# Kernel tuning notes

Hardware: AMD Instinct MI355X
Metric: run time of the kernel (lower is better)

Reference implementation:

```python
import jax, jax.numpy as jnp
import numpy as np

N, M, K = 100000, 20000, 640000   # nodes, hyperedges, incidence entries
IN_DIM, HID = 256, 128
L = 3                             # hdn_layers
EPS = 1e-5                        # BatchNorm1d eps


def setup_inputs() -> dict:
    key = jax.random.key(0)
    ks = jax.random.split(key, 8)
    init = lambda k, shape, fan: jax.random.normal(k, shape, jnp.float32) * (1.0 / np.sqrt(fan))
    return {
        "X": jax.random.normal(ks[0], (N, IN_DIM), jnp.float32),
        "node_idx": jax.random.randint(ks[1], (K,), 0, N, jnp.int32),
        "edge_idx": jax.random.randint(ks[2], (K,), 0, M, jnp.int32),
        "hyperedge_weight": jax.random.uniform(ks[3], (M,), jnp.float32),
        "W_up": init(ks[4], (IN_DIM, HID), IN_DIM),
        "b_up": jnp.zeros((HID,), jnp.float32),
        "bn_gamma": jnp.ones((L, HID), jnp.float32),
        "bn_beta": jnp.zeros((L, HID), jnp.float32),
        "W_conv": init(ks[5], (L, HID, HID), HID),
        "b_conv": jnp.zeros((L, HID), jnp.float32),
        "W_gate": init(ks[6], (L, HID, 1), HID),
        "b_gate": jnp.zeros((L, 1), jnp.float32),  # init_bias = 0.0
    }


def _batchnorm(x, gamma, beta):
    # BatchNorm1d in training mode: batch stats, biased variance
    mu = jnp.mean(x, axis=0)
    var = jnp.mean(jnp.square(x - mu), axis=0)
    return (x - mu) * jax.lax.rsqrt(var + EPS) * gamma + beta


def _hypergraph_conv(x, W, b, node_idx, edge_idx, w):
    # PyG HypergraphConv (heads=1): X' = D^{-1} H B^{-1} H^T (X W) + b,
    # where D_i = sum_{e ni i} w_e (w enters only via D, per PyG source),
    # B_e = |e|. 1/0 -> 0 as in PyG.
    x = x @ W                                                   # [N, HID]
    D = jax.ops.segment_sum(w[edge_idx], node_idx, num_segments=N)
    Dinv = jnp.where(D > 0, 1.0 / D, 0.0)
    Bdeg = jax.ops.segment_sum(jnp.ones((K,), x.dtype), edge_idx, num_segments=M)
    Binv = jnp.where(Bdeg > 0, 1.0 / Bdeg, 0.0)
    e = jax.ops.segment_sum(x[node_idx], edge_idx, num_segments=M) * Binv[:, None]   # edge feats [M, HID]
    out = jax.ops.segment_sum(e[edge_idx], node_idx, num_segments=N) * Dinv[:, None]  # node feats [N, HID]
    return out + b


def reference(X, node_idx, edge_idx, hyperedge_weight, W_up, b_up,
              bn_gamma, bn_beta, W_conv, b_conv, W_gate, b_gate):
    # lin_up: Linear + ReLU (in_dim != hidden_dim)
    x = jax.nn.relu(X @ W_up + b_up)
    identity = x
    for i in range(L):
        h = jax.nn.relu(_hypergraph_conv(
            _batchnorm(x, bn_gamma[i], bn_beta[i]),
            W_conv[i], b_conv[i], node_idx, edge_idx, hyperedge_weight))
        gate = jax.nn.sigmoid(x @ W_gate[i] + b_gate[i])        # [N, 1]
        x = x + h * gate
    # hidden_dim == out_dim -> lin_down = Identity, conv_down = Identity
    return (x + identity) + x
```

## Files before the change

kernel.cpp:

```cpp
#include <hip/hip_runtime.h>
#include <math.h>

#define NN 100000
#define MM 20000
#define KINC 640000
#define INDIM 256
#define HIDDIM 128
#define EPSBN 1e-5f

typedef __attribute__((ext_vector_type(4))) float f32x4;
typedef __attribute__((ext_vector_type(8))) short bf16x8;
typedef unsigned short ushort_t;

__device__ inline unsigned f2bf_bits(float f) {
  unsigned u = __float_as_uint(f);
  return u + 0x7FFFu + ((u >> 16) & 1u);
}
__device__ inline void split1(float f, ushort_t& hi, ushort_t& lo) {
  unsigned rh = f2bf_bits(f) & 0xFFFF0000u;
  hi = (ushort_t)(rh >> 16);
  float d = f - __uint_as_float(rh);
  lo = (ushort_t)(f2bf_bits(d) >> 16);
}


__global__ void hist_kernel(const int* __restrict__ nidx, const int* __restrict__ eidx,
                            const float* __restrict__ w, int* __restrict__ ecnt,
                            int* __restrict__ ncnt, float* __restrict__ D) {
  int stride = gridDim.x * blockDim.x;
  for (int k = blockIdx.x * blockDim.x + threadIdx.x; k < KINC; k += stride) {
    int e = eidx[k], n = nidx[k];
    atomicAdd(&ecnt[e], 1);
    atomicAdd(&ncnt[n], 1);
    atomicAdd(&D[n], w[e]);
  }
}

__global__ void base_kernel(const int* __restrict__ cnt, int* __restrict__ ptr,
                            int* __restrict__ pend, float* __restrict__ binv,
                            int* __restrict__ counter, int len) {
  int i = blockIdx.x * blockDim.x + threadIdx.x;
  int lane = threadIdx.x & 63;
  int v = (i < len) ? cnt[i] : 0;
  int s = v;
  #pragma unroll
  for (int off = 1; off < 64; off <<= 1) {
    int t = __shfl_up(s, off);
    if (lane >= off) s += t;
  }
  int total = __shfl(s, 63);
  int base = 0;
  if (lane == 0) base = atomicAdd(counter, total);
  base = __shfl(base, 0);
  if (i < len) {
    ptr[i] = base + s - v;
    pend[i] = base + s;
    if (binv) binv[i] = (v > 0) ? 1.0f / (float)v : 0.0f;
  }
}

__global__ void fill_kernel(const int* __restrict__ nidx, const int* __restrict__ eidx,
                            int* __restrict__ ecnt, int* __restrict__ ncnt,
                            const int* __restrict__ eptr, const int* __restrict__ nptr,
                            int* __restrict__ enodes, int* __restrict__ nedges) {
  int stride = gridDim.x * blockDim.x;
  for (int k = blockIdx.x * blockDim.x + threadIdx.x; k < KINC; k += stride) {
    int e = eidx[k], n = nidx[k];
    int pe = atomicSub(&ecnt[e], 1) - 1;
    enodes[eptr[e] + pe] = n;
    int pn = atomicSub(&ncnt[n], 1) - 1;
    nedges[nptr[n] + pn] = e;
  }
}

__global__ void dinv_kernel(float* __restrict__ D) {
  int i = blockIdx.x * blockDim.x + threadIdx.x;
  if (i < NN) { float d = D[i]; D[i] = (d > 0.0f) ? 1.0f / d : 0.0f; }
}

__global__ void wsplit_up_kernel(const float* __restrict__ W, ushort_t* __restrict__ Th,
                                 ushort_t* __restrict__ Tl) {
  int idx = blockIdx.x * 256 + threadIdx.x;
  int c = idx >> 8, k = idx & 255;
  ushort_t h, l;
  split1(W[k * HIDDIM + c], h, l);
  Th[c * INDIM + k] = h;
  Tl[c * INDIM + k] = l;
}

__global__ void prep_kernel(const float* __restrict__ stats, const float* __restrict__ gamma,
    const float* __restrict__ beta, const float* __restrict__ Wc,
    ushort_t* __restrict__ Th, ushort_t* __restrict__ Tl, float* __restrict__ bp) {
  __shared__ float al[128], cc[128];
  int t = threadIdx.x;
  if (t < 128) {
    float mu = stats[t] * (1.0f / NN);
    float var = fmaxf(stats[128 + t] * (1.0f / NN) - mu * mu, 0.0f);
    float a = gamma[t] * rsqrtf(var + EPSBN);
    al[t] = a;
    cc[t] = beta[t] - mu * a;
  }
  __syncthreads();
  for (int idx = t; idx < 128 * 128; idx += 256) {
    int c = idx >> 7, k = idx & 127;
    ushort_t h, l;
    split1(al[k] * Wc[k * 128 + c], h, l);
    Th[c * 128 + k] = h;
    Tl[c * 128 + k] = l;
  }
  if (t < 128) {
    float b = 0.f;
    for (int k = 0; k < 128; ++k) b = fmaf(cc[k], Wc[k * 128 + t], b);
    bp[t] = b;
  }
}

template<int KDIM, bool RELU, bool DUP>
__global__ __launch_bounds__(256) void mgemm_kernel(const float* __restrict__ A,
    const ushort_t* __restrict__ BTh, const ushort_t* __restrict__ BTl,
    const float* __restrict__ bias, float* __restrict__ out, float* __restrict__ out2,
    int nrows) {
  const int lane = threadIdx.x & 63;
  const int wv = threadIdx.x >> 6;
  const int m = lane & 15;
  const int kg = lane >> 4;
  const int r0 = blockIdx.x * 128;
  const int rt0 = r0 + wv * 16;
  const int rt1 = r0 + 64 + wv * 16;

  f32x4 acc0[8], acc1[8];
  #pragma unroll
  for (int ct = 0; ct < 8; ++ct) {
    acc0[ct] = (f32x4){0.f, 0.f, 0.f, 0.f};
    acc1[ct] = (f32x4){0.f, 0.f, 0.f, 0.f};
  }
  float bv[8];
  #pragma unroll
  for (int ct = 0; ct < 8; ++ct) bv[ct] = bias[ct * 16 + m];

  const int row0 = rt0 + m, row1 = rt1 + m;
  const bool v0 = row0 < nrows, v1 = row1 < nrows;
  const float* a0p = A + (size_t)row0 * KDIM + kg * 8;
  const float* a1p = A + (size_t)row1 * KDIM + kg * 8;

  for (int ks = 0; ks < KDIM; ks += 32) {
    float a0[8] = {0, 0, 0, 0, 0, 0, 0, 0}, a1[8] = {0, 0, 0, 0, 0, 0, 0, 0};
    if (v0) {
      *(float4*)(a0) = *(const float4*)(a0p + ks);
      *(float4*)(a0 + 4) = *(const float4*)(a0p + ks + 4);
    }
    if (v1) {
      *(float4*)(a1) = *(const float4*)(a1p + ks);
      *(float4*)(a1 + 4) = *(const float4*)(a1p + ks + 4);
    }
    bf16x8 a0h, a0l, a1h, a1l;
    #pragma unroll
    for (int j = 0; j < 8; ++j) {
      ushort_t h, l;
      split1(a0[j], h, l); a0h[j] = (short)h; a0l[j] = (short)l;
      split1(a1[j], h, l); a1h[j] = (short)h; a1l[j] = (short)l;
    }
    #pragma unroll
    for (int ct = 0; ct < 8; ++ct) {
      size_t bo = (size_t)(ct * 16 + m) * KDIM + ks + kg * 8;
      bf16x8 bh = *(const bf16x8*)(BTh + bo);
      bf16x8 bl = *(const bf16x8*)(BTl + bo);
      acc0[ct] = __builtin_amdgcn_mfma_f32_16x16x32_bf16(a0h, bh, acc0[ct], 0, 0, 0);
      acc0[ct] = __builtin_amdgcn_mfma_f32_16x16x32_bf16(a0l, bh, acc0[ct], 0, 0, 0);
      acc0[ct] = __builtin_amdgcn_mfma_f32_16x16x32_bf16(a0h, bl, acc0[ct], 0, 0, 0);
      acc1[ct] = __builtin_amdgcn_mfma_f32_16x16x32_bf16(a1h, bh, acc1[ct], 0, 0, 0);
      acc1[ct] = __builtin_amdgcn_mfma_f32_16x16x32_bf16(a1l, bh, acc1[ct], 0, 0, 0);
      acc1[ct] = __builtin_amdgcn_mfma_f32_16x16x32_bf16(a1h, bl, acc1[ct], 0, 0, 0);
    }
  }
  #pragma unroll
  for (int ct = 0; ct < 8; ++ct) {
    #pragma unroll
    for (int j = 0; j < 4; ++j) {
      int r = rt0 + kg * 4 + j;
      if (r < nrows) {
        float v = acc0[ct][j] + bv[ct];
        if (RELU) v = fmaxf(v, 0.0f);
        out[(size_t)r * HIDDIM + ct * 16 + m] = v;
        if (DUP) out2[(size_t)r * HIDDIM + ct * 16 + m] = v;
      }
      r = rt1 + kg * 4 + j;
      if (r < nrows) {
        float v = acc1[ct][j] + bv[ct];
        if (RELU) v = fmaxf(v, 0.0f);
        out[(size_t)r * HIDDIM + ct * 16 + m] = v;
        if (DUP) out2[(size_t)r * HIDDIM + ct * 16 + m] = v;
      }
    }
  }
}

__global__ __launch_bounds__(256) void stats_kernel(const float* __restrict__ x,
    float* __restrict__ out, int n) {
  __shared__ float lsum[128], lsq[128];
  int t = threadIdx.x;
  int lane = t & 63, wv = t >> 6;
  if (t < 128) { lsum[t] = 0.f; lsq[t] = 0.f; }
  __syncthreads();
  float sx = 0, sy = 0, qx = 0, qy = 0;
  const float2* x2 = (const float2*)x;
  for (int r = blockIdx.x * 4 + wv; r < n; r += gridDim.x * 4) {
    float2 v = x2[(size_t)r * 64 + lane];
    sx += v.x; sy += v.y; qx += v.x * v.x; qy += v.y * v.y;
  }
  atomicAdd(&lsum[2 * lane], sx);
  atomicAdd(&lsum[2 * lane + 1], sy);
  atomicAdd(&lsq[2 * lane], qx);
  atomicAdd(&lsq[2 * lane + 1], qy);
  __syncthreads();
  if (t < 128) {
    atomicAdd(&out[t], lsum[t]);
    atomicAdd(&out[128 + t], lsq[t]);
  }
}

__global__ __launch_bounds__(256) void edge_agg_kernel(const float* __restrict__ xw,
    const int* __restrict__ eptr, const int* __restrict__ pend,
    const int* __restrict__ enodes, const float* __restrict__ binv,
    float* __restrict__ e2) {
  int gw = (blockIdx.x * 256 + threadIdx.x) >> 6;
  int lane = threadIdx.x & 63;
  int e = __builtin_amdgcn_readfirstlane(gw);
  if (e >= MM) return;
  int p0 = eptr[e], p1 = pend[e];
  const float2* xw2 = (const float2*)xw;
  float ax = 0, ay = 0, bx = 0, by = 0;
  int j = p0;
  for (; j + 2 <= p1; j += 2) {
    int n0 = enodes[j], n1 = enodes[j + 1];
    float2 v0 = xw2[(size_t)n0 * 64 + lane];
    float2 v1 = xw2[(size_t)n1 * 64 + lane];
    ax += v0.x; ay += v0.y; bx += v1.x; by += v1.y;
  }
  if (j < p1) {
    int n0 = enodes[j];
    float2 v0 = xw2[(size_t)n0 * 64 + lane];
    ax += v0.x; ay += v0.y;
  }
  float bi = binv[e];
  float2 r; r.x = (ax + bx) * bi; r.y = (ay + by) * bi;
  ((float2*)e2)[(size_t)e * 64 + lane] = r;
}

template<bool LAST>
__global__ __launch_bounds__(256) void node_agg_kernel(const float* __restrict__ e2,
    const int* __restrict__ nptr, const int* __restrict__ pend,
    const int* __restrict__ nedges, const float* __restrict__ dinv,
    const float* __restrict__ bconv, const float* __restrict__ wgate,
    const float* __restrict__ bgate, const float* __restrict__ x,
    float* __restrict__ xout, const float* __restrict__ idres, float* __restrict__ fout,
    float* __restrict__ stats_out) {
  __shared__ float ls[256];
  int t = threadIdx.x;
  int lane = t & 63, wv = t >> 6;
  ls[t] = 0.f;
  __syncthreads();
  float sx = 0, sy = 0, qx = 0, qy = 0;
  const float2* e22 = (const float2*)e2;
  for (int nid0 = blockIdx.x * 4 + wv; nid0 < NN; nid0 += gridDim.x * 4) {
    int nid = __builtin_amdgcn_readfirstlane(nid0);
    int p0 = nptr[nid], p1 = pend[nid];
    float ax = 0, ay = 0;
    for (int j = p0; j < p1; ++j) {
      int e = nedges[j];
      float2 v = e22[(size_t)e * 64 + lane];
      ax += v.x; ay += v.y;
    }
    float di = dinv[nid];
    float2 xv = ((const float2*)x)[(size_t)nid * 64 + lane];
    float2 wg = ((const float2*)wgate)[lane];
    float part = xv.x * wg.x + xv.y * wg.y;
    #pragma unroll
    for (int off = 32; off >= 1; off >>= 1) part += __shfl_xor(part, off);
    float g = 1.0f / (1.0f + expf(-(part + bgate[0])));
    float2 bc = ((const float2*)bconv)[lane];
    float hx = fmaxf(fmaf(ax, di, bc.x), 0.0f);
    float hy = fmaxf(fmaf(ay, di, bc.y), 0.0f);
    float2 xn; xn.x = fmaf(hx, g, xv.x); xn.y = fmaf(hy, g, xv.y);
    if (LAST) {
      float2 idv = ((const float2*)idres)[(size_t)nid * 64 + lane];
      float2 o; o.x = 2.0f * xn.x + idv.x; o.y = 2.0f * xn.y + idv.y;
      ((float2*)fout)[(size_t)nid * 64 + lane] = o;
    } else {
      ((float2*)xout)[(size_t)nid * 64 + lane] = xn;
      sx += xn.x; sy += xn.y; qx += xn.x * xn.x; qy += xn.y * xn.y;
    }
  }
  if (!LAST) {
    atomicAdd(&ls[2 * lane], sx);
    atomicAdd(&ls[2 * lane + 1], sy);
    atomicAdd(&ls[128 + 2 * lane], qx);
    atomicAdd(&ls[128 + 2 * lane + 1], qy);
    __syncthreads();
    atomicAdd(&stats_out[t], ls[t]);
  }
}

extern "C" void kernel_launch(void* const* d_in, const int* in_sizes, int n_in,
                              void* d_out, int out_size, void* d_ws, size_t ws_size,
                              hipStream_t stream) {
  const float* X      = (const float*)d_in[0];
  const int*   nidx   = (const int*)d_in[1];
  const int*   eidx   = (const int*)d_in[2];
  const float* hw     = (const float*)d_in[3];
  const float* W_up   = (const float*)d_in[4];
  const float* b_up   = (const float*)d_in[5];
  const float* gamma  = (const float*)d_in[6];
  const float* beta   = (const float*)d_in[7];
  const float* W_conv = (const float*)d_in[8];
  const float* b_conv = (const float*)d_in[9];
  const float* W_gate = (const float*)d_in[10];
  const float* b_gate = (const float*)d_in[11];
  float* out = (float*)d_out;

  char* ws = (char*)d_ws;
  size_t off = 0;
  auto alloc = [&](size_t bytes) -> void* {
    void* p = ws + off;
    off = (off + bytes + 255) & ~(size_t)255;
    return p;
  };
  float* D     = (float*)alloc((size_t)NN * 4);
  int*   ecnt  = (int*)alloc((size_t)MM * 4);
  int*   ncnt  = (int*)alloc((size_t)NN * 4);
  int*   ctrs  = (int*)alloc(256);
  float* stats = (float*)alloc(3 * 256 * 4);
  size_t zero_bytes = off;
  int*   eptr   = (int*)alloc((size_t)MM * 4);
  int*   epend  = (int*)alloc((size_t)MM * 4);
  int*   nptr   = (int*)alloc((size_t)NN * 4);
  int*   npend  = (int*)alloc((size_t)NN * 4);
  float* Binv   = (float*)alloc((size_t)MM * 4);
  int*   enodes = (int*)alloc((size_t)KINC * 4);
  int*   nedges = (int*)alloc((size_t)KINC * 4);
  float* x      = (float*)alloc((size_t)NN * HIDDIM * 4);
  float* idr    = (float*)alloc((size_t)NN * HIDDIM * 4);
  float* e2     = (float*)alloc((size_t)MM * HIDDIM * 4);
  ushort_t* WupTh = (ushort_t*)alloc((size_t)HIDDIM * INDIM * 2);
  ushort_t* WupTl = (ushort_t*)alloc((size_t)HIDDIM * INDIM * 2);
  ushort_t* WTh   = (ushort_t*)alloc((size_t)HIDDIM * HIDDIM * 2);
  ushort_t* WTl   = (ushort_t*)alloc((size_t)HIDDIM * HIDDIM * 2);
  float* bp     = (float*)alloc((size_t)HIDDIM * 4);
  float* xw     = out;

  hipMemsetAsync(d_ws, 0, zero_bytes, stream);
  hist_kernel<<<512, 256, 0, stream>>>(nidx, eidx, hw, ecnt, ncnt, D);
  base_kernel<<<(MM + 255) / 256, 256, 0, stream>>>(ecnt, eptr, epend, Binv, ctrs + 0, MM);
  base_kernel<<<(NN + 255) / 256, 256, 0, stream>>>(ncnt, nptr, npend, nullptr, ctrs + 1, NN);
  fill_kernel<<<512, 256, 0, stream>>>(nidx, eidx, ecnt, ncnt, eptr, nptr, enodes, nedges);
  dinv_kernel<<<(NN + 255) / 256, 256, 0, stream>>>(D);
  wsplit_up_kernel<<<128, 256, 0, stream>>>(W_up, WupTh, WupTl);

  mgemm_kernel<INDIM, true, true><<<(NN + 127) / 128, 256, 0, stream>>>(
      X, WupTh, WupTl, b_up, x, idr, NN);
  stats_kernel<<<256, 256, 0, stream>>>(x, stats + 0, NN);

  for (int i = 0; i < 3; ++i) {
    prep_kernel<<<1, 256, 0, stream>>>(stats + i * 256, gamma + i * 128, beta + i * 128,
                                       W_conv + (size_t)i * 128 * 128, WTh, WTl, bp);
    mgemm_kernel<HIDDIM, false, false><<<(NN + 127) / 128, 256, 0, stream>>>(
        x, WTh, WTl, bp, xw, nullptr, NN);
    edge_agg_kernel<<<MM / 4, 256, 0, stream>>>(xw, eptr, epend, enodes, Binv, e2);
    if (i < 2)
      node_agg_kernel<false><<<1280, 256, 0, stream>>>(e2, nptr, npend, nedges, D,
          b_conv + i * 128, W_gate + i * 128, b_gate + i, x, x, nullptr, nullptr,
          stats + (i + 1) * 256);
    else
      node_agg_kernel<true><<<1280, 256, 0, stream>>>(e2, nptr, npend, nedges, D,
          b_conv + i * 128, W_gate + i * 128, b_gate + i, x, nullptr, idr, out, nullptr);
  }
}
```

Baseline: 1.042 ms.

## Pre-swizzle split weights into MFMA fragment order and stage them in LDS

Weight hi/lo bf16 splits are now written in MFMA fragment order, so each lane's 8-element operand is contiguous. The GEMM copies 64-K chunks of these fragments into shared memory before use instead of re-reading them from global memory per tile. The operands are swapped so the output tile is transposed, which lets each lane store rows as float4. Blocks now cover 64 rows instead of 128 with 4-block occupancy hints, trading per-wave A-row reuse for more parallelism and adding block barriers.

```diff
diff --git a/kernel.cpp b/kernel.cpp
--- a/kernel.cpp
+++ b/kernel.cpp
@@ -78,19 +78,26 @@
   if (i < NN) { float d = D[i]; D[i] = (d > 0.0f) ? 1.0f / d : 0.0f; }
 }
 
-__global__ void wsplit_up_kernel(const float* __restrict__ W, ushort_t* __restrict__ Th,
-                                 ushort_t* __restrict__ Tl) {
-  int idx = blockIdx.x * 256 + threadIdx.x;
-  int c = idx >> 8, k = idx & 255;
-  ushort_t h, l;
-  split1(W[k * HIDDIM + c], h, l);
-  Th[c * INDIM + k] = h;
-  Tl[c * INDIM + k] = l;
+__global__ void wsplit_up_kernel(const float* __restrict__ W, ushort_t* __restrict__ Fh,
+                                 ushort_t* __restrict__ Fl) {
+  int g = blockIdx.x * 256 + threadIdx.x;
+  int ln = g & 63;
+  int ct = (g >> 6) & 7;
+  int ksg = g >> 9;
+  int c = ct * 16 + (ln & 15);
+  int k0 = ksg * 32 + (ln >> 4) * 8;
+  #pragma unroll
+  for (int j = 0; j < 8; ++j) {
+    ushort_t h, l;
+    split1(W[(size_t)(k0 + j) * HIDDIM + c], h, l);
+    Fh[(size_t)g * 8 + j] = h;
+    Fl[(size_t)g * 8 + j] = l;
+  }
 }
 
 __global__ void prep_kernel(const float* __restrict__ stats, const float* __restrict__ gamma,
     const float* __restrict__ beta, const float* __restrict__ Wc,
-    ushort_t* __restrict__ Th, ushort_t* __restrict__ Tl, float* __restrict__ bp) {
+    ushort_t* __restrict__ Fh, ushort_t* __restrict__ Fl, float* __restrict__ bp) {
   __shared__ float al[128], cc[128];
   int t = threadIdx.x;
   if (t < 128) {
@@ -101,12 +108,19 @@
     cc[t] = beta[t] - mu * a;
   }
   __syncthreads();
-  for (int idx = t; idx < 128 * 128; idx += 256) {
-    int c = idx >> 7, k = idx & 127;
-    ushort_t h, l;
-    split1(al[k] * Wc[k * 128 + c], h, l);
-    Th[c * 128 + k] = h;
-    Tl[c * 128 + k] = l;
+  for (int g = t; g < 2048; g += 256) {
+    int ln = g & 63;
+    int ct = (g >> 6) & 7;
+    int ksg = g >> 9;
+    int c = ct * 16 + (ln & 15);
+    int k0 = ksg * 32 + (ln >> 4) * 8;
+    #pragma unroll
+    for (int j = 0; j < 8; ++j) {
+      ushort_t h, l;
+      split1(al[k0 + j] * Wc[(k0 + j) * 128 + c], h, l);
+      Fh[(size_t)g * 8 + j] = h;
+      Fl[(size_t)g * 8 + j] = l;
+    }
   }
   if (t < 128) {
     float b = 0.f;
@@ -116,81 +130,81 @@
 }
 
 template<int KDIM, bool RELU, bool DUP>
-__global__ __launch_bounds__(256) void mgemm_kernel(const float* __restrict__ A,
-    const ushort_t* __restrict__ BTh, const ushort_t* __restrict__ BTl,
+__global__ __launch_bounds__(256, 4) void mgemm_kernel(const float* __restrict__ A,
+    const ushort_t* __restrict__ WFh, const ushort_t* __restrict__ WFl,
     const float* __restrict__ bias, float* __restrict__ out, float* __restrict__ out2,
     int nrows) {
-  const int lane = threadIdx.x & 63;
-  const int wv = threadIdx.x >> 6;
+  __shared__ ushort_t Bls[16384];
+  const int t = threadIdx.x;
+  const int lane = t & 63;
+  const int wv = t >> 6;
   const int m = lane & 15;
   const int kg = lane >> 4;
-  const int r0 = blockIdx.x * 128;
-  const int rt0 = r0 + wv * 16;
-  const int rt1 = r0 + 64 + wv * 16;
-
-  f32x4 acc0[8], acc1[8];
+  const int rt = blockIdx.x * 64 + wv * 16;
+
+  f32x4 acc[8];
   #pragma unroll
-  for (int ct = 0; ct < 8; ++ct) {
-    acc0[ct] = (f32x4){0.f, 0.f, 0.f, 0.f};
-    acc1[ct] = (f32x4){0.f, 0.f, 0.f, 0.f};
-  }
-  float bv[8];
-  #pragma unroll
-  for (int ct = 0; ct < 8; ++ct) bv[ct] = bias[ct * 16 + m];
-
-  const int row0 = rt0 + m, row1 = rt1 + m;
-  const bool v0 = row0 < nrows, v1 = row1 < nrows;
+  for (int ct = 0; ct < 8; ++ct) acc[ct] = (f32x4){0.f, 0.f, 0.f, 0.f};
+
+  const int row0 = rt + m;
+  const bool v0 = row0 < nrows;
   const float* a0p = A + (size_t)row0 * KDIM + kg * 8;
-  const float* a1p = A + (size_t)row1 * KDIM + kg * 8;
-
-  for (int ks = 0; ks < KDIM; ks += 32) {
-    float a0[8] = {0, 0, 0, 0, 0, 0, 0, 0}, a1[8] = {0, 0, 0, 0, 0, 0, 0, 0};
-    if (v0) {
-      *(float4*)(a0) = *(const float4*)(a0p + ks);
-      *(float4*)(a0 + 4) = *(const float4*)(a0p + ks + 4);
-    }
-    if (v1) {
-      *(float4*)(a1) = *(const float4*)(a1p + ks);
-      *(float4*)(a1 + 4) = *(const float4*)(a1p + ks + 4);
-    }
-    bf16x8 a0h, a0l, a1h, a1l;
-    #pragma unroll
-    for (int j = 0; j < 8; ++j) {
-      ushort_t h, l;
-      split1(a0[j], h, l); a0h[j] = (short)h; a0l[j] = (short)l;
-      split1(a1[j], h, l); a1h[j] = (short)h; a1l[j] = (short)l;
-    }
+
+  for (int c2 = 0; c2 < KDIM / 64; ++c2) {
+    if (c2) __syncthreads();
+    const uint4* sh = (const uint4*)(WFh + c2 * 8192);
+    const uint4* sl = (const uint4*)(WFl + c2 * 8192);
+    uint4* dh = (uint4*)Bls;
+    uint4* dl = (uint4*)(Bls + 8192);
+    #pragma unroll
+    for (int i = 0; i < 4; ++i) {
+      dh[i * 256 + t] = sh[i * 256 + t];
+      dl[i * 256 + t] = sl[i * 256 + t];
+    }
+    __syncthreads();
+    #pragma unroll
+    for (int ks2 = 0; ks2 < 2; ++ks2) {
+      int kof = c2 * 64 + ks2 * 32;
+      float a0[8] = {0, 0, 0, 0, 0, 0, 0, 0};
+      if (v0) {
+        *(float4*)(a0) = *(const float4*)(a0p + kof);
+        *(float4*)(a0 + 4) = *(const float4*)(a0p + kof + 4);
+      }
+      bf16x8 a0h, a0l;
+      #pragma unroll
+      for (int j = 0; j < 8; ++j) {
+        ushort_t h, l;
+        split1(a0[j], h, l);
+        a0h[j] = (short)h;
+        a0l[j] = (short)l;
+      }
+      #pragma unroll
+      for (int ct = 0; ct < 8; ++ct) {
+        int fo = ((ks2 * 8 + ct) * 64 + lane) * 8;
+        bf16x8 bh = *(const bf16x8*)(Bls + fo);
+        bf16x8 bl = *(const bf16x8*)(Bls + 8192 + fo);
+        acc[ct] = __builtin_amdgcn_mfma_f32_16x16x32_bf16(bh, a0h, acc[ct], 0, 0, 0);
+        acc[ct] = __builtin_amdgcn_mfma_f32_16x16x32_bf16(bl, a0h, acc[ct], 0, 0, 0);
+        acc[ct] = __builtin_amdgcn_mfma_f32_16x16x32_bf16(bh, a0l, acc[ct], 0, 0, 0);
+      }
+    }
+  }
+  if (row0 < nrows) {
+    float* o = out + (size_t)row0 * HIDDIM;
     #pragma unroll
     for (int ct = 0; ct < 8; ++ct) {
-      size_t bo = (size_t)(ct * 16 + m) * KDIM + ks + kg * 8;
-      bf16x8 bh = *(const bf16x8*)(BTh + bo);
-      bf16x8 bl = *(const bf16x8*)(BTl + bo);
-      acc0[ct] = __builtin_amdgcn_mfma_f32_16x16x32_bf16(a0h, bh, acc0[ct], 0, 0, 0);
-      acc0[ct] = __builtin_amdgcn_mfma_f32_16x16x32_bf16(a0l, bh, acc0[ct], 0, 0, 0);
-      acc0[ct] = __builtin_amdgcn_mfma_f32_16x16x32_bf16(a0h, bl, acc0[ct], 0, 0, 0);
-      acc1[ct] = __builtin_amdgcn_mfma_f32_16x16x32_bf16(a1h, bh, acc1[ct], 0, 0, 0);
-      acc1[ct] = __builtin_amdgcn_mfma_f32_16x16x32_bf16(a1l, bh, acc1[ct], 0, 0, 0);
-      acc1[ct] = __builtin_amdgcn_mfma_f32_16x16x32_bf16(a1h, bl, acc1[ct], 0, 0, 0);
-    }
-  }
-  #pragma unroll
-  for (int ct = 0; ct < 8; ++ct) {
-    #pragma unroll
-    for (int j = 0; j < 4; ++j) {
-      int r = rt0 + kg * 4 + j;
-      if (r < nrows) {
-        float v = acc0[ct][j] + bv[ct];
-        if (RELU) v = fmaxf(v, 0.0f);
-        out[(size_t)r * HIDDIM + ct * 16 + m] = v;
-        if (DUP) out2[(size_t)r * HIDDIM + ct * 16 + m] = v;
+      float4 b4 = ((const float4*)bias)[ct * 4 + kg];
+      float4 v;
+      v.x = acc[ct][0] + b4.x;
+      v.y = acc[ct][1] + b4.y;
+      v.z = acc[ct][2] + b4.z;
+      v.w = acc[ct][3] + b4.w;
+      if (RELU) {
+        v.x = fmaxf(v.x, 0.f); v.y = fmaxf(v.y, 0.f);
+        v.z = fmaxf(v.z, 0.f); v.w = fmaxf(v.w, 0.f);
       }
-      r = rt1 + kg * 4 + j;
-      if (r < nrows) {
-        float v = acc1[ct][j] + bv[ct];
-        if (RELU) v = fmaxf(v, 0.0f);
-        out[(size_t)r * HIDDIM + ct * 16 + m] = v;
-        if (DUP) out2[(size_t)r * HIDDIM + ct * 16 + m] = v;
-      }
+      *(float4*)(o + ct * 16 + kg * 4) = v;
+      if (DUP) *(float4*)(out2 + (size_t)row0 * HIDDIM + ct * 16 + kg * 4) = v;
     }
   }
 }
@@ -341,10 +355,10 @@
   float* x      = (float*)alloc((size_t)NN * HIDDIM * 4);
   float* idr    = (float*)alloc((size_t)NN * HIDDIM * 4);
   float* e2     = (float*)alloc((size_t)MM * HIDDIM * 4);
-  ushort_t* WupTh = (ushort_t*)alloc((size_t)HIDDIM * INDIM * 2);
-  ushort_t* WupTl = (ushort_t*)alloc((size_t)HIDDIM * INDIM * 2);
-  ushort_t* WTh   = (ushort_t*)alloc((size_t)HIDDIM * HIDDIM * 2);
-  ushort_t* WTl   = (ushort_t*)alloc((size_t)HIDDIM * HIDDIM * 2);
+  ushort_t* WupFh = (ushort_t*)alloc((size_t)HIDDIM * INDIM * 2);
+  ushort_t* WupFl = (ushort_t*)alloc((size_t)HIDDIM * INDIM * 2);
+  ushort_t* WFh   = (ushort_t*)alloc((size_t)HIDDIM * HIDDIM * 2);
+  ushort_t* WFl   = (ushort_t*)alloc((size_t)HIDDIM * HIDDIM * 2);
   float* bp     = (float*)alloc((size_t)HIDDIM * 4);
   float* xw     = out;
 
@@ -354,17 +368,17 @@
   base_kernel<<<(NN + 255) / 256, 256, 0, stream>>>(ncnt, nptr, npend, nullptr, ctrs + 1, NN);
   fill_kernel<<<512, 256, 0, stream>>>(nidx, eidx, ecnt, ncnt, eptr, nptr, enodes, nedges);
   dinv_kernel<<<(NN + 255) / 256, 256, 0, stream>>>(D);
-  wsplit_up_kernel<<<128, 256, 0, stream>>>(W_up, WupTh, WupTl);
-
-  mgemm_kernel<INDIM, true, true><<<(NN + 127) / 128, 256, 0, stream>>>(
-      X, WupTh, WupTl, b_up, x, idr, NN);
+  wsplit_up_kernel<<<16, 256, 0, stream>>>(W_up, WupFh, WupFl);
+
+  mgemm_kernel<INDIM, true, true><<<(NN + 63) / 64, 256, 0, stream>>>(
+      X, WupFh, WupFl, b_up, x, idr, NN);
   stats_kernel<<<256, 256, 0, stream>>>(x, stats + 0, NN);
 
   for (int i = 0; i < 3; ++i) {
     prep_kernel<<<1, 256, 0, stream>>>(stats + i * 256, gamma + i * 128, beta + i * 128,
-                                       W_conv + (size_t)i * 128 * 128, WTh, WTl, bp);
-    mgemm_kernel<HIDDIM, false, false><<<(NN + 127) / 128, 256, 0, stream>>>(
-        x, WTh, WTl, bp, xw, nullptr, NN);
+                                       W_conv + (size_t)i * 128 * 128, WFh, WFl, bp);
+    mgemm_kernel<HIDDIM, false, false><<<(NN + 63) / 64, 256, 0, stream>>>(
+        x, WFh, WFl, bp, xw, nullptr, NN);
     edge_agg_kernel<<<MM / 4, 256, 0, stream>>>(xw, eptr, epend, enodes, Binv, e2);
     if (i < 2)
       node_agg_kernel<false><<<1280, 256, 0, stream>>>(e2, nptr, npend, nedges, D,
```

After: 924.7 us. 1.13x faster.
